# Performance work log

Hardware: AMD Instinct MI355X
Metric: run time of the kernel (lower is better)

The kernel has to match this reference:

```python
import jax, jax.numpy as jnp
import numpy as np

B, N, M, F1, F2 = 8, 128, 256, 256, 256


def setup_inputs() -> dict:
    key = jax.random.key(0)
    k = jax.random.split(key, 6)
    s = 1.0 / np.sqrt(F1)
    return {
        "x": jax.random.normal(k[0], (B, N, F1), dtype=jnp.float32),
        "y": jax.random.normal(k[1], (B, M, F2), dtype=jnp.float32),
        "U_w": jax.random.normal(k[2], (F2, F1), dtype=jnp.float32) * s,
        "U_b": jax.random.normal(k[3], (F2,), dtype=jnp.float32) * s,
        "W_w": jax.random.normal(k[4], (1, F2), dtype=jnp.float32) * (1.0 / np.sqrt(F2)),
        "W_b": jax.random.normal(k[5], (1,), dtype=jnp.float32) * (1.0 / np.sqrt(F2)),
    }


def reference(x, y, U_w, U_b, W_w, W_b):
    # poolAttn path (default). dropout=0 -> identity.
    u = jnp.einsum('bnf,gf->bng', x, U_w) + U_b          # [B,N,F2]
    # broadcast bilinear: tanh(u[:,:,None,:] * y[:,None,:,:]) -> [B,N,M,F2]
    a = jnp.tanh(u[:, :, None, :] * y[:, None, :, :])
    alpha = jnp.einsum('bnmf,f->bnm', a, W_w[0]) + W_b[0]  # [B,N,M]
    # x attention: max over M, softmax over N
    xw = jax.nn.softmax(alpha.max(axis=2), axis=1)         # [B,N]
    x_pooled = jnp.einsum('bnf,bn->bf', x, xw)             # [B,F1]
    # y attention: max over N, softmax over M
    yw = jax.nn.softmax(alpha.max(axis=1), axis=1)         # [B,M]
    y_pooled = jnp.einsum('bm,bmf->bf', yw, y)             # [B,F2]
    return jnp.concatenate([x_pooled, y_pooled], axis=1)   # [B,F1+F2]
```

## Files before the change

### kernel.cpp

```cpp
#include <hip/hip_runtime.h>
#include <math.h>

#define B_ 8
#define N_ 128
#define M_ 256
#define F_ 256

#define LOG2E2 2.8853900817779268f

__global__ __launch_bounds__(256) void k1_lite(const float* __restrict__ x,
                                               const float* __restrict__ Uw,
                                               const float* __restrict__ Ub,
                                               float* __restrict__ u) {
  const int g  = threadIdx.x;
  const int r0 = blockIdx.x * 4;
  const float* __restrict__ uwr = Uw + (size_t)g * F_;
  const float* __restrict__ xr  = x + (size_t)r0 * F_;

  float a0 = 0.f, a1 = 0.f, a2 = 0.f, a3 = 0.f;
#pragma unroll 4
  for (int f = 0; f < F_; f += 4) {
    const float4 wv = *(const float4*)&uwr[f];
    const float4 x0 = *(const float4*)&xr[0 * F_ + f];
    const float4 x1 = *(const float4*)&xr[1 * F_ + f];
    const float4 x2 = *(const float4*)&xr[2 * F_ + f];
    const float4 x3 = *(const float4*)&xr[3 * F_ + f];
    a0 = fmaf(wv.x, x0.x, a0); a0 = fmaf(wv.y, x0.y, a0);
    a0 = fmaf(wv.z, x0.z, a0); a0 = fmaf(wv.w, x0.w, a0);
    a1 = fmaf(wv.x, x1.x, a1); a1 = fmaf(wv.y, x1.y, a1);
    a1 = fmaf(wv.z, x1.z, a1); a1 = fmaf(wv.w, x1.w, a1);
    a2 = fmaf(wv.x, x2.x, a2); a2 = fmaf(wv.y, x2.y, a2);
    a2 = fmaf(wv.z, x2.z, a2); a2 = fmaf(wv.w, x2.w, a2);
    a3 = fmaf(wv.x, x3.x, a3); a3 = fmaf(wv.y, x3.y, a3);
    a3 = fmaf(wv.z, x3.z, a3); a3 = fmaf(wv.w, x3.w, a3);
  }
  const float ubv = Ub[g];
  u[(size_t)(r0 + 0) * F_ + g] = (a0 + ubv) * LOG2E2;
  u[(size_t)(r0 + 1) * F_ + g] = (a1 + ubv) * LOG2E2;
  u[(size_t)(r0 + 2) * F_ + g] = (a2 + ubv) * LOG2E2;
  u[(size_t)(r0 + 3) * F_ + g] = (a3 + ubv) * LOG2E2;
}

__global__ void k2_alpha(const float* __restrict__ u,
                         const float* __restrict__ y,
                         const float* __restrict__ Ww,
                         float* __restrict__ rminp,
                         float* __restrict__ cminp) {
  __shared__ float us[8][F_];
  __shared__ float red[8][8][64];
  __shared__ float sm[8][64];

  const int tid  = threadIdx.x;
  const int mg   = blockIdx.x;
  const int ns   = blockIdx.y;
  const int b    = blockIdx.z;
  const int n0   = ns * 8;
  const int m0   = mg * 64;
  const int lane = tid & 63;
  const int w    = tid >> 6;
  const int fc   = __builtin_amdgcn_readfirstlane(w);

  {
    const int r = tid >> 6, c = (tid & 63) * 4;
    *(float4*)&us[r][c] =
        *(const float4*)&u[(size_t)(b * N_ + n0 + r) * F_ + c];
  }

  float4 yv[8];
  float4 wwv[8];
  {
    const float* yr = y + ((size_t)(b * M_ + m0 + lane)) * F_ + fc * 32;
    const float* wr = Ww + fc * 32;
#pragma unroll
    for (int j = 0; j < 8; ++j) {
      yv[j]  = *(const float4*)&yr[4 * j];
      wwv[j] = *(const float4*)&wr[4 * j];
    }
  }
  __syncthreads();

#define QUAD(nn, j, S0, S1)                                                   \
  do {                                                                        \
    const float4 uv = *(const float4*)&us[nn][fc * 32 + 4 * (j)];             \
    const float t0 = uv.x * yv[j].x;                                          \
    const float t1 = uv.y * yv[j].y;                                          \
    const float t2 = uv.z * yv[j].z;                                          \
    const float t3 = uv.w * yv[j].w;                                          \
    const float d0 = 1.f + __builtin_amdgcn_exp2f(t0);                        \
    const float d1 = 1.f + __builtin_amdgcn_exp2f(t1);                        \
    const float d2 = 1.f + __builtin_amdgcn_exp2f(t2);                        \
    const float d3 = 1.f + __builtin_amdgcn_exp2f(t3);                        \
    const float n01 = fmaf(wwv[j].x, d1, wwv[j].y * d0);                      \
    const float n23 = fmaf(wwv[j].z, d3, wwv[j].w * d2);                      \
    S0 = fmaf(n01, __builtin_amdgcn_rcpf(d0 * d1), S0);                       \
    S1 = fmaf(n23, __builtin_amdgcn_rcpf(d2 * d3), S1);                       \
  } while (0)

#define DO_N(nn, A)                                                                      \
  do {                                                                                   \
    float s0 = 0.f, s1 = 0.f;                                                            \
    QUAD(nn, 0, s0, s1); QUAD(nn, 1, s0, s1); QUAD(nn, 2, s0, s1); QUAD(nn, 3, s0, s1);  \
    QUAD(nn, 4, s0, s1); QUAD(nn, 5, s0, s1); QUAD(nn, 6, s0, s1); QUAD(nn, 7, s0, s1);  \
    A = s0 + s1;                                                                         \
  } while (0)

  float a0, a1, a2, a3, a4, a5, a6, a7;
  DO_N(0, a0); DO_N(1, a1); DO_N(2, a2); DO_N(3, a3);
  DO_N(4, a4); DO_N(5, a5); DO_N(6, a6); DO_N(7, a7);
#undef DO_N
#undef QUAD

  red[0][fc][lane] = a0; red[1][fc][lane] = a1;
  red[2][fc][lane] = a2; red[3][fc][lane] = a3;
  red[4][fc][lane] = a4; red[5][fc][lane] = a5;
  red[6][fc][lane] = a6; red[7][fc][lane] = a7;
  __syncthreads();

  float S = 0.f;
#pragma unroll
  for (int k = 0; k < 8; ++k) S += red[w][k][lane];

  float r = S;
#pragma unroll
  for (int s = 32; s; s >>= 1) r = fminf(r, __shfl_xor(r, s));
  if (lane == 0) rminp[((size_t)b * 4 + mg) * N_ + n0 + w] = r;

  sm[w][lane] = S;
  __syncthreads();
  if (w == 0) {
    float c = sm[0][lane];
#pragma unroll
    for (int k = 1; k < 8; ++k) c = fminf(c, sm[k][lane]);
    cminp[((size_t)b * 16 + ns) * M_ + m0 + lane] = c;
  }
}

__global__ __launch_bounds__(256) void kb_final(
    const float* __restrict__ x, const float* __restrict__ y,
    const float* __restrict__ rminp, const float* __restrict__ cminp,
    float* __restrict__ out) {
  const int b    = blockIdx.x;
  const int task = blockIdx.y;
  const int fq   = blockIdx.z;
  const int tid  = threadIdx.x;
  const int w    = tid >> 6;
  __shared__ float wgt[M_];
  __shared__ float redv[4];
  __shared__ float part[4][64];

  if (task == 0) {
    float rv = -INFINITY;
    if (tid < N_) {
      float v = INFINITY;
#pragma unroll
      for (int mg = 0; mg < 4; ++mg)
        v = fminf(v, rminp[((size_t)b * 4 + mg) * N_ + tid]);
      rv = -2.f * v;
    }
    float m1 = rv;
#pragma unroll
    for (int s = 32; s; s >>= 1) m1 = fmaxf(m1, __shfl_xor(m1, s));
    if ((tid & 63) == 0) redv[w] = m1;
    __syncthreads();
    m1 = fmaxf(fmaxf(redv[0], redv[1]), fmaxf(redv[2], redv[3]));
    __syncthreads();
    const float e1 = (tid < N_) ? __expf(rv - m1) : 0.f;
    float s1 = e1;
#pragma unroll
    for (int s = 32; s; s >>= 1) s1 += __shfl_xor(s1, s);
    if ((tid & 63) == 0) redv[w] = s1;
    __syncthreads();
    s1 = redv[0] + redv[1] + redv[2] + redv[3];
    if (tid < N_) wgt[tid] = e1 / s1;
    __syncthreads();

    const int f = fq * 64 + (tid & 63);
    float acc = 0.f;
#pragma unroll 8
    for (int n = w; n < N_; n += 4)
      acc = fmaf(wgt[n], x[(size_t)(b * N_ + n) * F_ + f], acc);
    part[w][tid & 63] = acc;
    __syncthreads();
    if (tid < 64)
      out[b * (2 * F_) + fq * 64 + tid] =
          part[0][tid] + part[1][tid] + part[2][tid] + part[3][tid];
  } else {
    float cv;
    {
      float c = INFINITY;
#pragma unroll
      for (int ns = 0; ns < 16; ++ns)
        c = fminf(c, cminp[((size_t)b * 16 + ns) * M_ + tid]);
      cv = -2.f * c;
    }
    float m2 = cv;
#pragma unroll
    for (int s = 32; s; s >>= 1) m2 = fmaxf(m2, __shfl_xor(m2, s));
    if ((tid & 63) == 0) redv[w] = m2;
    __syncthreads();
    m2 = fmaxf(fmaxf(redv[0], redv[1]), fmaxf(redv[2], redv[3]));
    __syncthreads();
    const float e2 = __expf(cv - m2);
    float s2 = e2;
#pragma unroll
    for (int s = 32; s; s >>= 1) s2 += __shfl_xor(s2, s);
    if ((tid & 63) == 0) redv[w] = s2;
    __syncthreads();
    s2 = redv[0] + redv[1] + redv[2] + redv[3];
    wgt[tid] = e2 / s2;
    __syncthreads();

    const int f = fq * 64 + (tid & 63);
    float acc = 0.f;
#pragma unroll 8
    for (int m = w; m < M_; m += 4)
      acc = fmaf(wgt[m], y[(size_t)(b * M_ + m) * F_ + f], acc);
    part[w][tid & 63] = acc;
    __syncthreads();
    if (tid < 64)
      out[b * (2 * F_) + F_ + fq * 64 + tid] =
          part[0][tid] + part[1][tid] + part[2][tid] + part[3][tid];
  }
}

extern "C" void kernel_launch(void* const* d_in, const int* in_sizes, int n_in,
                              void* d_out, int out_size, void* d_ws, size_t ws_size,
                              hipStream_t stream) {
  (void)in_sizes; (void)n_in; (void)out_size; (void)ws_size;
  const float* x  = (const float*)d_in[0];
  const float* y  = (const float*)d_in[1];
  const float* Uw = (const float*)d_in[2];
  const float* Ub = (const float*)d_in[3];
  const float* Ww = (const float*)d_in[4];

  float* u     = (float*)d_ws;
  float* rminp = u + B_ * N_ * F_;
  float* cminp = rminp + B_ * 4 * N_;
  float* outp  = (float*)d_out;

  k1_lite<<<dim3((B_ * N_) / 4), 256, 0, stream>>>(x, Uw, Ub, u);
  k2_alpha<<<dim3(4, 16, B_), 512, 0, stream>>>(u, y, Ww, rminp, cminp);
  kb_final<<<dim3(B_, 2, 4), 256, 0, stream>>>(x, y, rminp, cminp, outp);
}
```

Before: 35.05 us.

## Fuse final softmax-pooling into alpha kernel via last-block atomic ticket

Removes the separate kb_final launch. Each k2 block increments a per-batch counter after writing its partial minima, and the last of the 64 blocks per batch computes both softmaxes and the pooled outputs. The counter is reset inside k1. This trades one kernel launch and its gap for a serialized tail, where a single 512-thread block per batch does all the pooling work that was previously spread over 8 blocks. It also relies on threadfence plus atomic ordering being correct.

Measured after the change: 110.8 us. +216.1%, slower.

```diff
diff --git a/kernel.cpp b/kernel.cpp
--- a/kernel.cpp
+++ b/kernel.cpp
@@ -11,7 +11,10 @@
 __global__ __launch_bounds__(256) void k1_lite(const float* __restrict__ x,
                                                const float* __restrict__ Uw,
                                                const float* __restrict__ Ub,
-                                               float* __restrict__ u) {
+                                               float* __restrict__ u,
+                                               unsigned* __restrict__ counter) {
+  if (blockIdx.x == 0 && threadIdx.x < 8) counter[threadIdx.x] = 0u;
+
   const int g  = threadIdx.x;
   const int r0 = blockIdx.x * 4;
   const float* __restrict__ uwr = Uw + (size_t)g * F_;
@@ -41,14 +44,22 @@
   u[(size_t)(r0 + 3) * F_ + g] = (a3 + ubv) * LOG2E2;
 }
 
-__global__ void k2_alpha(const float* __restrict__ u,
-                         const float* __restrict__ y,
-                         const float* __restrict__ Ww,
-                         float* __restrict__ rminp,
-                         float* __restrict__ cminp) {
+__global__ void k2kb(const float* __restrict__ u,
+                     const float* __restrict__ y,
+                     const float* __restrict__ Ww,
+                     const float* __restrict__ x,
+                     float* __restrict__ rminp,
+                     float* __restrict__ cminp,
+                     unsigned* __restrict__ counter,
+                     float* __restrict__ out) {
   __shared__ float us[8][F_];
   __shared__ float red[8][8][64];
   __shared__ float sm[8][64];
+  __shared__ float xw[N_];
+  __shared__ float yw[M_];
+  __shared__ float bred[8];
+  __shared__ float part[2][256];
+  __shared__ unsigned ticket_s;
 
   const int tid  = threadIdx.x;
   const int mg   = blockIdx.x;
@@ -133,94 +144,87 @@
     for (int k = 1; k < 8; ++k) c = fminf(c, sm[k][lane]);
     cminp[((size_t)b * 16 + ns) * M_ + m0 + lane] = c;
   }
-}
-
-__global__ __launch_bounds__(256) void kb_final(
-    const float* __restrict__ x, const float* __restrict__ y,
-    const float* __restrict__ rminp, const float* __restrict__ cminp,
-    float* __restrict__ out) {
-  const int b    = blockIdx.x;
-  const int task = blockIdx.y;
-  const int fq   = blockIdx.z;
-  const int tid  = threadIdx.x;
-  const int w    = tid >> 6;
-  __shared__ float wgt[M_];
-  __shared__ float redv[4];
-  __shared__ float part[4][64];
-
-  if (task == 0) {
-    float rv = -INFINITY;
-    if (tid < N_) {
-      float v = INFINITY;
-#pragma unroll
-      for (int mg = 0; mg < 4; ++mg)
-        v = fminf(v, rminp[((size_t)b * 4 + mg) * N_ + tid]);
-      rv = -2.f * v;
-    }
-    float m1 = rv;
-#pragma unroll
-    for (int s = 32; s; s >>= 1) m1 = fmaxf(m1, __shfl_xor(m1, s));
-    if ((tid & 63) == 0) redv[w] = m1;
-    __syncthreads();
-    m1 = fmaxf(fmaxf(redv[0], redv[1]), fmaxf(redv[2], redv[3]));
-    __syncthreads();
-    const float e1 = (tid < N_) ? __expf(rv - m1) : 0.f;
-    float s1 = e1;
-#pragma unroll
-    for (int s = 32; s; s >>= 1) s1 += __shfl_xor(s1, s);
-    if ((tid & 63) == 0) redv[w] = s1;
-    __syncthreads();
-    s1 = redv[0] + redv[1] + redv[2] + redv[3];
-    if (tid < N_) wgt[tid] = e1 / s1;
-    __syncthreads();
-
-    const int f = fq * 64 + (tid & 63);
-    float acc = 0.f;
-#pragma unroll 8
-    for (int n = w; n < N_; n += 4)
-      acc = fmaf(wgt[n], x[(size_t)(b * N_ + n) * F_ + f], acc);
-    part[w][tid & 63] = acc;
-    __syncthreads();
-    if (tid < 64)
-      out[b * (2 * F_) + fq * 64 + tid] =
-          part[0][tid] + part[1][tid] + part[2][tid] + part[3][tid];
-  } else {
-    float cv;
-    {
-      float c = INFINITY;
-#pragma unroll
-      for (int ns = 0; ns < 16; ++ns)
-        c = fminf(c, cminp[((size_t)b * 16 + ns) * M_ + tid]);
-      cv = -2.f * c;
-    }
-    float m2 = cv;
-#pragma unroll
-    for (int s = 32; s; s >>= 1) m2 = fmaxf(m2, __shfl_xor(m2, s));
-    if ((tid & 63) == 0) redv[w] = m2;
-    __syncthreads();
-    m2 = fmaxf(fmaxf(redv[0], redv[1]), fmaxf(redv[2], redv[3]));
-    __syncthreads();
-    const float e2 = __expf(cv - m2);
-    float s2 = e2;
-#pragma unroll
-    for (int s = 32; s; s >>= 1) s2 += __shfl_xor(s2, s);
-    if ((tid & 63) == 0) redv[w] = s2;
-    __syncthreads();
-    s2 = redv[0] + redv[1] + redv[2] + redv[3];
-    wgt[tid] = e2 / s2;
-    __syncthreads();
-
-    const int f = fq * 64 + (tid & 63);
-    float acc = 0.f;
-#pragma unroll 8
-    for (int m = w; m < M_; m += 4)
-      acc = fmaf(wgt[m], y[(size_t)(b * M_ + m) * F_ + f], acc);
-    part[w][tid & 63] = acc;
-    __syncthreads();
-    if (tid < 64)
-      out[b * (2 * F_) + F_ + fq * 64 + tid] =
-          part[0][tid] + part[1][tid] + part[2][tid] + part[3][tid];
-  }
+
+  __threadfence();
+  __syncthreads();
+  if (tid == 0) ticket_s = atomicAdd(&counter[b], 1u);
+  __syncthreads();
+  if (ticket_s != 63u) return;
+  __threadfence();
+
+  float rv = -INFINITY;
+  if (tid < N_) {
+    float v = INFINITY;
+#pragma unroll
+    for (int mg2 = 0; mg2 < 4; ++mg2)
+      v = fminf(v, rminp[((size_t)b * 4 + mg2) * N_ + tid]);
+    rv = -2.f * v;
+  }
+  float m1 = rv;
+#pragma unroll
+  for (int s = 32; s; s >>= 1) m1 = fmaxf(m1, __shfl_xor(m1, s));
+  if (lane == 0) bred[w] = m1;
+  __syncthreads();
+  m1 = bred[0];
+#pragma unroll
+  for (int k = 1; k < 8; ++k) m1 = fmaxf(m1, bred[k]);
+  __syncthreads();
+  const float e1 = (tid < N_) ? __expf(rv - m1) : 0.f;
+  float s1 = e1;
+#pragma unroll
+  for (int s = 32; s; s >>= 1) s1 += __shfl_xor(s1, s);
+  if (lane == 0) bred[w] = s1;
+  __syncthreads();
+  s1 = bred[0] + bred[1] + bred[2] + bred[3] +
+       bred[4] + bred[5] + bred[6] + bred[7];
+  if (tid < N_) xw[tid] = e1 / s1;
+  __syncthreads();
+
+  float cv = -INFINITY;
+  if (tid < M_) {
+    float c = INFINITY;
+#pragma unroll
+    for (int k = 0; k < 16; ++k)
+      c = fminf(c, cminp[((size_t)b * 16 + k) * M_ + tid]);
+    cv = -2.f * c;
+  }
+  float m2 = cv;
+#pragma unroll
+  for (int s = 32; s; s >>= 1) m2 = fmaxf(m2, __shfl_xor(m2, s));
+  if (lane == 0) bred[w] = m2;
+  __syncthreads();
+  m2 = bred[0];
+#pragma unroll
+  for (int k = 1; k < 8; ++k) m2 = fmaxf(m2, bred[k]);
+  __syncthreads();
+  const float e2 = (tid < M_) ? __expf(cv - m2) : 0.f;
+  float s2 = e2;
+#pragma unroll
+  for (int s = 32; s; s >>= 1) s2 += __shfl_xor(s2, s);
+  if (lane == 0) bred[w] = s2;
+  __syncthreads();
+  s2 = bred[0] + bred[1] + bred[2] + bred[3] +
+       bred[4] + bred[5] + bred[6] + bred[7];
+  if (tid < M_) yw[tid] = e2 / s2;
+  __syncthreads();
+
+  const int q = tid >> 8;
+  const int f = tid & 255;
+  float accx = 0.f;
+#pragma unroll 4
+  for (int n = q; n < N_; n += 2)
+    accx = fmaf(xw[n], x[(size_t)(b * N_ + n) * F_ + f], accx);
+  part[q][f] = accx;
+  __syncthreads();
+  if (tid < 256) out[b * (2 * F_) + f] = part[0][f] + part[1][f];
+  __syncthreads();
+  float accy = 0.f;
+#pragma unroll 4
+  for (int mm = q; mm < M_; mm += 2)
+    accy = fmaf(yw[mm], y[(size_t)(b * M_ + mm) * F_ + f], accy);
+  part[q][f] = accy;
+  __syncthreads();
+  if (tid < 256) out[b * (2 * F_) + F_ + f] = part[0][f] + part[1][f];
 }
 
 extern "C" void kernel_launch(void* const* d_in, const int* in_sizes, int n_in,
@@ -233,12 +237,13 @@
   const float* Ub = (const float*)d_in[3];
   const float* Ww = (const float*)d_in[4];
 
-  float* u     = (float*)d_ws;
-  float* rminp = u + B_ * N_ * F_;
-  float* cminp = rminp + B_ * 4 * N_;
-  float* outp  = (float*)d_out;
-
-  k1_lite<<<dim3((B_ * N_) / 4), 256, 0, stream>>>(x, Uw, Ub, u);
-  k2_alpha<<<dim3(4, 16, B_), 512, 0, stream>>>(u, y, Ww, rminp, cminp);
-  kb_final<<<dim3(B_, 2, 4), 256, 0, stream>>>(x, y, rminp, cminp, outp);
+  float* u        = (float*)d_ws;
+  float* rminp    = u + B_ * N_ * F_;
+  float* cminp    = rminp + B_ * 4 * N_;
+  unsigned* cnt   = (unsigned*)(cminp + B_ * 16 * M_);
+  float* outp     = (float*)d_out;
+
+  k1_lite<<<dim3((B_ * N_) / 4), 256, 0, stream>>>(x, Uw, Ub, u, cnt);
+  k2kb<<<dim3(4, 16, B_), 512, 0, stream>>>(u, y, Ww, x, rminp, cminp, cnt,
+                                            outp);
 }
```
